# Kernel tuning notes

Measured on AMD Instinct MI355X. Metric: run time of the kernel, lower is better.

Reference implementation:

```python
import jax, jax.numpy as jnp
import numpy as np

N = 50000    # nodes
E = 800000   # edges (avg degree 16)
B = 256      # graphs in the batch (static for segment ops)
H = 128      # feature / hidden width (channels[-2])
NL = 4       # LSTM layers in Set2Set
PS = 4       # Set2Set processing steps
OUT = 2      # channels[-1]


def _bn(h, g, b):
    # BatchNorm1d with batch statistics (training-mode math, biased variance)
    m = h.mean(0)
    v = jnp.mean((h - m) ** 2, 0)
    return (h - m) * jax.lax.rsqrt(v + 1e-5) * g + b


def _gin(x, src, dst, W1, b1, ga1, be1, W2, b2, ga2, be2):
    # GINConv, eps=0: out = MLP(x + sum_{j->i} x_j)
    agg = jax.ops.segment_sum(x[src], dst, num_segments=x.shape[0])
    h = x + agg
    h = jax.nn.relu(_bn(h @ W1.T + b1, ga1, be1))
    h = jax.nn.relu(_bn(h @ W2.T + b2, ga2, be2))
    return h


def _set2set(x, batch, Wih0, Whh0, b0, WihR, WhhR, bR):
    hs = [jnp.zeros((B, H), x.dtype)] * NL
    cs = [jnp.zeros((B, H), x.dtype)] * NL
    q_star = jnp.zeros((B, 2 * H), x.dtype)
    for _ in range(PS):
        inp = q_star
        nhs, ncs = [], []
        for l in range(NL):  # stacked LSTM cells, seq-len 1 per step
            Wih = Wih0 if l == 0 else WihR[l - 1]
            Whh = Whh0 if l == 0 else WhhR[l - 1]
            bb = b0 if l == 0 else bR[l - 1]
            gates = inp @ Wih.T + hs[l] @ Whh.T + bb
            i, f, g, o = jnp.split(gates, 4, axis=-1)  # torch gate order i,f,g,o
            c = jax.nn.sigmoid(f) * cs[l] + jax.nn.sigmoid(i) * jnp.tanh(g)
            h = jax.nn.sigmoid(o) * jnp.tanh(c)
            nhs.append(h); ncs.append(c)
            inp = h
        hs, cs = nhs, ncs
        q = inp  # (B, H) top-layer hidden
        # per-graph segment softmax attention
        e = jnp.sum(x * q[batch], -1)                        # (N,)
        m = jax.ops.segment_max(e, batch, num_segments=B)
        ee = jnp.exp(e - m[batch])
        s = jax.ops.segment_sum(ee, batch, num_segments=B)
        a = ee / s[batch]
        r = jax.ops.segment_sum(a[:, None] * x, batch, num_segments=B)  # (B, H)
        q_star = jnp.concatenate([q, r], -1)
    return q_star


def setup_inputs() -> dict:
    key = jax.random.key(0)
    ks = jax.random.split(key, 16)

    def w(k, shape):
        return jax.random.normal(k, shape, jnp.float32) * 0.05

    d = {}
    d["x"] = jax.random.normal(ks[0], (N, H), jnp.float32)
    d["edge_index"] = jax.random.randint(ks[1], (2, E), 0, N, dtype=jnp.int32)
    d["batch"] = jnp.sort(jax.random.randint(ks[2], (N,), 0, B, dtype=jnp.int32))
    for i, g in enumerate(("g0", "g1")):
        kk = jax.random.split(ks[3 + i], 2)
        d[g + "_W1"] = w(kk[0], (H, H)); d[g + "_b1"] = jnp.zeros((H,), jnp.float32)
        d[g + "_gamma1"] = jnp.ones((H,), jnp.float32); d[g + "_beta1"] = jnp.zeros((H,), jnp.float32)
        d[g + "_W2"] = w(kk[1], (H, H)); d[g + "_b2"] = jnp.zeros((H,), jnp.float32)
        d[g + "_gamma2"] = jnp.ones((H,), jnp.float32); d[g + "_beta2"] = jnp.zeros((H,), jnp.float32)
    d["Wih0"] = w(ks[6], (4 * H, 2 * H))
    d["Whh0"] = w(ks[7], (4 * H, H))
    d["b0"] = jnp.zeros((4 * H,), jnp.float32)
    d["WihR"] = w(ks[8], (NL - 1, 4 * H, H))
    d["WhhR"] = w(ks[9], (NL - 1, 4 * H, H))
    d["bR"] = jnp.zeros((NL - 1, 4 * H), jnp.float32)
    d["lin_W"] = w(ks[10], (OUT, 2 * H))
    d["lin_b"] = jnp.zeros((OUT,), jnp.float32)
    return d


def reference(x, edge_index, batch,
              g0_W1, g0_b1, g0_gamma1, g0_beta1, g0_W2, g0_b2, g0_gamma2, g0_beta2,
              g1_W1, g1_b1, g1_gamma1, g1_beta1, g1_W2, g1_b2, g1_gamma2, g1_beta2,
              Wih0, Whh0, b0, WihR, WhhR, bR, lin_W, lin_b):
    src, dst = edge_index[0], edge_index[1]
    x = _gin(x, src, dst, g0_W1, g0_b1, g0_gamma1, g0_beta1, g0_W2, g0_b2, g0_gamma2, g0_beta2)
    x = _gin(x, src, dst, g1_W1, g1_b1, g1_gamma1, g1_beta1, g1_W2, g1_b2, g1_gamma2, g1_beta2)
    q = _set2set(x, batch, Wih0, Whh0, b0, WihR, WhhR, bR)
    # F.dropout(p=0.1) is identity in eval mode
    return q @ lin_W.T + lin_b
```

## Files before the change

### kernel.cpp

```cpp
#include <hip/hip_runtime.h>
#include <math.h>

#define NN 50000
#define EE 800000
#define BBG 256
#define HHC 128
#define SEG_CAP 448
#define ESC 512
#define NBIN 196
#define NBLK 196

typedef _Float16 half8 __attribute__((ext_vector_type(8)));
typedef _Float16 half4 __attribute__((ext_vector_type(4)));
typedef _Float16 half2v __attribute__((ext_vector_type(2)));
typedef float f32x4 __attribute__((ext_vector_type(4)));

#if defined(__has_builtin)
#if __has_builtin(__builtin_amdgcn_fdot2)
#define USE_FDOT2 1
#endif
#endif

__device__ __forceinline__ float fdot2f(half2v a, half2v b, float c) {
#ifdef USE_FDOT2
  return __builtin_amdgcn_fdot2(a, b, c, false);
#else
  return fmaf((float)a[0], (float)b[0], fmaf((float)a[1], (float)b[1], c));
#endif
}

__device__ __forceinline__ float fsigm(float x) {
  return __builtin_amdgcn_rcpf(1.f + __expf(-x));
}
__device__ __forceinline__ float ftanh(float x) {
  return 1.f - 2.f * __builtin_amdgcn_rcpf(1.f + __expf(2.f * x));
}

__device__ __forceinline__ float4 aff4(float4 v, float4 sc, float4 sh) {
  v.x = fmaxf(fmaf(v.x, sc.x, sh.x), 0.f);
  v.y = fmaxf(fmaf(v.y, sc.y, sh.y), 0.f);
  v.z = fmaxf(fmaf(v.z, sc.z, sh.z), 0.f);
  v.w = fmaxf(fmaf(v.w, sc.w, sh.w), 0.f);
  return v;
}

__global__ __launch_bounds__(256) void prep_all_kernel(
    const int* __restrict__ batch,
    const int* __restrict__ ei,
    const float* __restrict__ W0, const float* __restrict__ W1,
    const float* __restrict__ W2, const float* __restrict__ W3,
    const float* __restrict__ Wih0, const float* __restrict__ Whh0,
    const float* __restrict__ WihR, const float* __restrict__ WhhR,
    const float* __restrict__ b0, const float* __restrict__ bR,
    const float* __restrict__ xsrc,
    float* __restrict__ stats, int* __restrict__ gptr, int* __restrict__ partial,
    _Float16* __restrict__ ginWh, _Float16* __restrict__ WT0h,
    _Float16* __restrict__ WTRh, float* __restrict__ bc0, float* __restrict__ bcR,
    _Float16* __restrict__ x16a) {
  __shared__ int hist[NBIN];
  int blk = blockIdx.x, tid = threadIdx.x;
  if (blk == 0) {
    ((float4*)stats)[tid] = make_float4(0.f, 0.f, 0.f, 0.f);
    return;
  }
  if (blk <= 196) {
    int i = (blk - 1) * 256 + tid;
    if (i >= NN) return;
    int b = batch[i];
    int prev = (i == 0) ? -1 : batch[i - 1];
    for (int g = prev + 1; g <= b; ++g) gptr[g] = i;
    if (i == NN - 1) {
      for (int g = b + 1; g <= BBG; ++g) gptr[g] = NN;
    }
    return;
  }
  if (blk <= 392) {
    int b = blk - 197;
    if (tid < NBIN) hist[tid] = 0;
    __syncthreads();
    const int4* dst4 = (const int4*)(ei + EE);
#pragma unroll
    for (int c = 0; c < 4; ++c) {
      int idx = b * 1024 + c * 256 + tid;
      if (idx < EE / 4) {
        int4 d = dst4[idx];
        atomicAdd(&hist[d.x >> 8], 1);
        atomicAdd(&hist[d.y >> 8], 1);
        atomicAdd(&hist[d.z >> 8], 1);
        atomicAdd(&hist[d.w >> 8], 1);
      }
    }
    __syncthreads();
    if (tid < NBIN) partial[tid * NBLK + b] = hist[tid];
    return;
  }
  if (blk >= 2961) {
    int i = (blk - 2961) * 256 + tid;
    float4 v = ((const float4*)xsrc)[i];
    half4 h;
    h[0] = (_Float16)v.x; h[1] = (_Float16)v.y;
    h[2] = (_Float16)v.z; h[3] = (_Float16)v.w;
    ((half4*)x16a)[i] = h;
    return;
  }
  int idx = (blk - 393) * 256 + tid;
  if (idx < 65536) {
    int m = idx >> 14;
    int r = idx & 16383;
    const float* W = (m == 0) ? W0 : (m == 1) ? W1 : (m == 2) ? W2 : W3;
    ginWh[idx] = (_Float16)W[r];
  } else if (idx < 262144) {
    int t = idx - 65536;
    int k = t >> 9, op = t & 511;
    int j = op >> 2, g = op & 3;
    int row = g * 128 + j;
    float v = (k < 256) ? Wih0[row * 256 + k] : Whh0[row * 128 + (k - 256)];
    WT0h[((k >> 1) << 10) | (op << 1) | (k & 1)] = (_Float16)v;
  } else if (idx < 655360) {
    int t = idx - 262144;
    int l = t >> 17;
    int rem = t & 131071;
    int k = rem >> 9, op = rem & 511;
    int j = op >> 2, g = op & 3;
    int row = g * 128 + j;
    float v = (k < 128) ? WihR[((size_t)l * 512 + row) * 128 + k]
                        : WhhR[((size_t)l * 512 + row) * 128 + (k - 128)];
    WTRh[((size_t)l << 17) | ((k >> 1) << 10) | (op << 1) | (k & 1)] = (_Float16)v;
  } else {
    int t = idx - 655360;
    if (t < 512) {
      bc0[t] = b0[(t & 3) * 128 + (t >> 2)];
    } else {
      int u = t - 512;
      int l = u >> 9, op = u & 511;
      bcR[u] = bR[l * 512 + (op & 3) * 128 + (op >> 2)];
    }
  }
}


__global__ void scan_partials_kernel(const int* __restrict__ partial,
                                     int* __restrict__ block_base, int* __restrict__ total) {
  __shared__ int buf[256];
  int bin = blockIdx.x, tid = threadIdx.x;
  int v = (tid < NBLK) ? partial[bin * NBLK + tid] : 0;
  buf[tid] = v;
  __syncthreads();
  for (int off = 1; off < 256; off <<= 1) {
    int t = (tid >= off) ? buf[tid - off] : 0;
    __syncthreads();
    buf[tid] += t;
    __syncthreads();
  }
  if (tid < NBLK) block_base[bin * NBLK + tid] = buf[tid] - v;
  if (tid == 255) total[bin] = buf[255];
}

__global__ void scan_totals_kernel(const int* __restrict__ total, int* __restrict__ coarse_base) {
  __shared__ int buf[256];
  int tid = threadIdx.x;
  int v = (tid < NBIN) ? total[tid] : 0;
  buf[tid] = v;
  __syncthreads();
  for (int off = 1; off < 256; off <<= 1) {
    int t = (tid >= off) ? buf[tid - off] : 0;
    __syncthreads();
    buf[tid] += t;
    __syncthreads();
  }
  if (tid < NBIN) coarse_base[tid] = buf[tid] - v;
  if (tid == 255) coarse_base[NBIN] = buf[255];
}

__global__ __launch_bounds__(256) void bucket_scatter_kernel(const int* __restrict__ ei,
                                                             const int* __restrict__ coarse_base,
                                                             const int* __restrict__ block_base,
                                                             int* __restrict__ packed) {
  __shared__ int cursor[NBIN];
  int tid = threadIdx.x, b = blockIdx.x;
  if (tid < NBIN) cursor[tid] = coarse_base[tid] + block_base[tid * NBLK + b];
  __syncthreads();
  const int4* src4 = (const int4*)ei;
  const int4* dst4 = (const int4*)(ei + EE);
#pragma unroll
  for (int c = 0; c < 4; ++c) {
    int idx = b * 1024 + c * 256 + tid;
    if (idx < EE / 4) {
      int4 s = src4[idx];
      int4 d = dst4[idx];
      int p;
      p = atomicAdd(&cursor[d.x >> 8], 1); packed[p] = (s.x << 8) | (d.x & 255);
      p = atomicAdd(&cursor[d.y >> 8], 1); packed[p] = (s.y << 8) | (d.y & 255);
      p = atomicAdd(&cursor[d.z >> 8], 1); packed[p] = (s.z << 8) | (d.z & 255);
      p = atomicAdd(&cursor[d.w >> 8], 1); packed[p] = (s.w << 8) | (d.w & 255);
    }
  }
}

__global__ __launch_bounds__(256) void csr_finalize_kernel(const int* __restrict__ packed,
                                                           const int* __restrict__ coarse_base,
                                                           int* __restrict__ row_start,
                                                           int* __restrict__ csr) {
  __shared__ int fh[256];
  __shared__ int fb[256];
  int bin = blockIdx.x, tid = threadIdx.x;
  int e0 = coarse_base[bin], e1 = coarse_base[bin + 1];
  fh[tid] = 0;
  __syncthreads();
  for (int e = e0 + tid; e < e1; e += 256) atomicAdd(&fh[packed[e] & 255], 1);
  __syncthreads();
  int v = fh[tid];
  fb[tid] = v;
  __syncthreads();
  for (int off = 1; off < 256; off <<= 1) {
    int t = (tid >= off) ? fb[tid - off] : 0;
    __syncthreads();
    fb[tid] += t;
    __syncthreads();
  }
  int excl = fb[tid] - v;
  int node = bin * 256 + tid;
  if (node < NN) row_start[node] = e0 + excl;
  if (bin == NBIN - 1 && tid == 0) row_start[NN] = EE;
  __syncthreads();
  fb[tid] = excl;
  __syncthreads();
  for (int e = e0 + tid; e < e1; e += 256) {
    int p = packed[e];
    int pos = atomicAdd(&fb[p & 255], 1);
    csr[e0 + pos] = p >> 8;
  }
}

template <bool AFF>
__global__ __launch_bounds__(256) void gin_agg_kernel(
    const _Float16* __restrict__ x16, const int* __restrict__ row_start,
    const int* __restrict__ csr,
    const float* __restrict__ stats, const float* __restrict__ gamma,
    const float* __restrict__ beta, _Float16* __restrict__ outp) {
  __shared__ float sc_s[128], sh_s[128];
  if (AFF) {
    int tt = threadIdx.x;
    if (tt < 128) {
      const float invN = 1.0f / (float)NN;
      float mm = stats[tt] * invN;
      float vv = stats[128 + tt] * invN - mm * mm;
      float rs = rsqrtf(vv + 1e-5f);
      float sc = gamma[tt] * rs;
      sc_s[tt] = sc;
      sh_s[tt] = beta[tt] - mm * sc;
    }
    __syncthreads();
  }
  int node = blockIdx.x * 4 + (threadIdx.x >> 6);
  int lane = threadIdx.x & 63;
  int q = lane >> 4, t = lane & 15;
  const half8* xh8 = (const half8*)x16;
  float scv[8], shv[8];
  if (AFF) {
#pragma unroll
    for (int f = 0; f < 8; ++f) { scv[f] = sc_s[t * 8 + f]; shv[f] = sh_s[t * 8 + f]; }
  }
  int s0 = row_start[node], s1 = row_start[node + 1];
  float acc[8] = {0.f, 0.f, 0.f, 0.f, 0.f, 0.f, 0.f, 0.f};
  int cnt = s1 - s0;
  int mainEnd = s0 + (cnt & ~15);
  for (int j = s0; j < mainEnd; j += 16) {
    int i0 = csr[j + q + 0];
    int i1 = csr[j + q + 4];
    int i2 = csr[j + q + 8];
    int i3 = csr[j + q + 12];
    half8 h0 = xh8[(size_t)i0 * 16 + t];
    half8 h1 = xh8[(size_t)i1 * 16 + t];
    half8 h2 = xh8[(size_t)i2 * 16 + t];
    half8 h3 = xh8[(size_t)i3 * 16 + t];
    if (AFF) {
#pragma unroll
      for (int f = 0; f < 8; ++f) {
        acc[f] += fmaxf(fmaf((float)h0[f], scv[f], shv[f]), 0.f);
        acc[f] += fmaxf(fmaf((float)h1[f], scv[f], shv[f]), 0.f);
        acc[f] += fmaxf(fmaf((float)h2[f], scv[f], shv[f]), 0.f);
        acc[f] += fmaxf(fmaf((float)h3[f], scv[f], shv[f]), 0.f);
      }
    } else {
#pragma unroll
      for (int f = 0; f < 8; ++f) {
        acc[f] += ((float)h0[f] + (float)h1[f]) + ((float)h2[f] + (float)h3[f]);
      }
    }
  }
  for (int j = mainEnd + q; j < s1; j += 4) {
    int i = csr[j];
    half8 h = xh8[(size_t)i * 16 + t];
    if (AFF) {
#pragma unroll
      for (int f = 0; f < 8; ++f) acc[f] += fmaxf(fmaf((float)h[f], scv[f], shv[f]), 0.f);
    } else {
#pragma unroll
      for (int f = 0; f < 8; ++f) acc[f] += (float)h[f];
    }
  }
#pragma unroll
  for (int f = 0; f < 8; ++f) {
    acc[f] += __shfl_xor(acc[f], 16);
    acc[f] += __shfl_xor(acc[f], 32);
  }
  if (q == 0) {
    half8 selfh = xh8[(size_t)node * 16 + t];
    half8 hv;
#pragma unroll
    for (int f = 0; f < 8; ++f) {
      float sv = (float)selfh[f];
      if (AFF) sv = fmaxf(fmaf(sv, scv[f], shv[f]), 0.f);
      hv[f] = (_Float16)(acc[f] + sv);
    }
    ((half8*)outp)[(size_t)node * 16 + t] = hv;
  }
}

template <bool BN, bool AH>
__global__ __launch_bounds__(256) void gemm_gin_mfma_kernel(
    const float* __restrict__ A, const _Float16* __restrict__ A16,
    const _Float16* __restrict__ Wh,
    const float* __restrict__ bias,
    const float* __restrict__ stats, const float* __restrict__ gamma,
    const float* __restrict__ beta,
    float* __restrict__ C, _Float16* __restrict__ h16out,
    float* __restrict__ ssum, float* __restrict__ ssq) {
  __shared__ float bsc_s[128], bsh_s[128];
  int tid = threadIdx.x;
  if (BN) {
    if (tid < 128) {
      const float invN = 1.0f / (float)NN;
      float mm = stats[tid] * invN;
      float vv = stats[128 + tid] * invN - mm * mm;
      float rs = rsqrtf(vv + 1e-5f);
      float sc = gamma[tid] * rs;
      bsc_s[tid] = sc;
      bsh_s[tid] = beta[tid] - mm * sc;
    }
    __syncthreads();
  }
  int w = tid >> 6, l = tid & 63;
  int lr = l & 15, lg = l >> 4;
  int cb = w * 32;
  half8 bf0[4], bf1[4];
#pragma unroll
  for (int ks = 0; ks < 4; ++ks) {
    int k = ks * 32 + lg * 8;
    bf0[ks] = *(const half8*)(Wh + (size_t)(cb + lr) * 128 + k);
    bf1[ks] = *(const half8*)(Wh + (size_t)(cb + 16 + lr) * 128 + k);
  }
  float bv0 = bias[cb + lr], bv1 = bias[cb + 16 + lr];
  float ps0 = 0.f, pq0 = 0.f, ps1 = 0.f, pq1 = 0.f;
  int t0 = blockIdx.x * 4;
  for (int t = 0; t < 4; ++t) {
    int tile = t0 + t;
    if (tile >= 3125) break;
    int r = tile * 16 + lr;
    half8 af[4];
#pragma unroll
    for (int ks = 0; ks < 4; ++ks) {
      int k0 = ks * 32 + lg * 8;
      if constexpr (AH) {
        half8 ah = *(const half8*)(A16 + (size_t)r * 128 + k0);
        if constexpr (BN) {
          float4 s0 = *(const float4*)&bsc_s[k0];
          float4 s1 = *(const float4*)&bsc_s[k0 + 4];
          float4 h0 = *(const float4*)&bsh_s[k0];
          float4 h1 = *(const float4*)&bsh_s[k0 + 4];
          half8 o;
          o[0] = (_Float16)fmaxf(fmaf((float)ah[0], s0.x, h0.x), 0.f);
          o[1] = (_Float16)fmaxf(fmaf((float)ah[1], s0.y, h0.y), 0.f);
          o[2] = (_Float16)fmaxf(fmaf((float)ah[2], s0.z, h0.z), 0.f);
          o[3] = (_Float16)fmaxf(fmaf((float)ah[3], s0.w, h0.w), 0.f);
          o[4] = (_Float16)fmaxf(fmaf((float)ah[4], s1.x, h1.x), 0.f);
          o[5] = (_Float16)fmaxf(fmaf((float)ah[5], s1.y, h1.y), 0.f);
          o[6] = (_Float16)fmaxf(fmaf((float)ah[6], s1.z, h1.z), 0.f);
          o[7] = (_Float16)fmaxf(fmaf((float)ah[7], s1.w, h1.w), 0.f);
          af[ks] = o;
        } else {
          af[ks] = ah;
        }
      } else {
        float4 a0 = *(const float4*)(A + (size_t)r * 128 + k0);
        float4 a1 = *(const float4*)(A + (size_t)r * 128 + k0 + 4);
        if constexpr (BN) {
          float4 s0 = *(const float4*)&bsc_s[k0];
          float4 s1 = *(const float4*)&bsc_s[k0 + 4];
          float4 h0 = *(const float4*)&bsh_s[k0];
          float4 h1 = *(const float4*)&bsh_s[k0 + 4];
          a0 = aff4(a0, s0, h0);
          a1 = aff4(a1, s1, h1);
        }
        half8 o;
        o[0] = (_Float16)a0.x; o[1] = (_Float16)a0.y;
        o[2] = (_Float16)a0.z; o[3] = (_Float16)a0.w;
        o[4] = (_Float16)a1.x; o[5] = (_Float16)a1.y;
        o[6] = (_Float16)a1.z; o[7] = (_Float16)a1.w;
        af[ks] = o;
      }
    }
    f32x4 acc0 = {0.f, 0.f, 0.f, 0.f};
    f32x4 acc1 = {0.f, 0.f, 0.f, 0.f};
#pragma unroll
    for (int ks = 0; ks < 4; ++ks) {
      acc0 = __builtin_amdgcn_mfma_f32_16x16x32_f16(af[ks], bf0[ks], acc0, 0, 0, 0);
      acc1 = __builtin_amdgcn_mfma_f32_16x16x32_f16(af[ks], bf1[ks], acc1, 0, 0, 0);
    }
#pragma unroll
    for (int i = 0; i < 4; ++i) {
      int rr = tile * 16 + lg * 4 + i;
      float v0 = acc0[i] + bv0;
      float v1 = acc1[i] + bv1;
      if (C) {
        C[(size_t)rr * 128 + cb + lr] = v0;
        C[(size_t)rr * 128 + cb + 16 + lr] = v1;
      }
      if (h16out) {
        h16out[(size_t)rr * 128 + cb + lr] = (_Float16)v0;
        h16out[(size_t)rr * 128 + cb + 16 + lr] = (_Float16)v1;
      }
      ps0 += v0; pq0 += v0 * v0;
      ps1 += v1; pq1 += v1 * v1;
    }
  }
  ps0 += __shfl_xor(ps0, 16); ps0 += __shfl_xor(ps0, 32);
  pq0 += __shfl_xor(pq0, 16); pq0 += __shfl_xor(pq0, 32);
  ps1 += __shfl_xor(ps1, 16); ps1 += __shfl_xor(ps1, 32);
  pq1 += __shfl_xor(pq1, 16); pq1 += __shfl_xor(pq1, 32);
  if (lg == 0) {
    atomicAdd(&ssum[cb + lr], ps0);
    atomicAdd(&ssq[cb + lr], pq0);
    atomicAdd(&ssum[cb + 16 + lr], ps1);
    atomicAdd(&ssq[cb + 16 + lr], pq1);
  }
}

__global__ void __launch_bounds__(1024) set2set_kernel(
    const float* __restrict__ x, const int* __restrict__ gptr,
    const float* __restrict__ stats, const float* __restrict__ gamma,
    const float* __restrict__ beta,
    const _Float16* __restrict__ WT0h, const _Float16* __restrict__ WTRh,
    const float* __restrict__ bc0, const float* __restrict__ bcR,
    float* __restrict__ ebuf,
    const float* __restrict__ linW, const float* __restrict__ linb,
    float* __restrict__ out) {
  __shared__ half2v xs[SEG_CAP * 64];
  __shared__ float wpart[16][512];
  __shared__ half2v inp2[192];
  __shared__ float hcs[4][128];
  __shared__ float ccs[4][128];
  __shared__ float qst[256];
  __shared__ float es[ESC];
  __shared__ float bsc[128], bsh[128];
  __shared__ float wred[16];
  __shared__ float smax_s, ssum_s;
  __shared__ float fred[2][4];

  int g = blockIdx.x, tid = threadIdx.x;
  int w16 = tid >> 6, lane = tid & 63;

  if (tid < 128) {
    const float invN = 1.0f / (float)NN;
    float mm = stats[tid] * invN;
    float vv = stats[128 + tid] * invN - mm * mm;
    float rs = rsqrtf(vv + 1e-5f);
    float sc = gamma[tid] * rs;
    bsc[tid] = sc;
    bsh[tid] = beta[tid] - mm * sc;
#pragma unroll
    for (int l = 0; l < 4; ++l) { hcs[l][tid] = 0.f; ccs[l][tid] = 0.f; }
  }
  if (tid < 256) qst[tid] = 0.f;
  __syncthreads();

  int s0 = gptr[g], s1 = gptr[g + 1];
  int seg = s1 - s0;
  int ncache = seg < SEG_CAP ? seg : SEG_CAP;
  const float2* x2 = (const float2*)x;
  float sc0 = bsc[2 * lane], sc1 = bsc[2 * lane + 1];
  float sh0 = bsh[2 * lane], sh1 = bsh[2 * lane + 1];
  for (int n = w16; n < ncache; n += 16) {
    float2 v = x2[(size_t)(s0 + n) * 64 + lane];
    half2v h;
    h[0] = (_Float16)fmaxf(fmaf(v.x, sc0, sh0), 0.f);
    h[1] = (_Float16)fmaxf(fmaf(v.y, sc1, sh1), 0.f);
    xs[n * 64 + lane] = h;
  }
  __syncthreads();

  int s_ = tid >> 6, cg = tid & 63;

  for (int step = 0; step < 4; ++step) {
    for (int cell = 0; cell < 4; ++cell) {
      const _Float16* WTh; const float* bias; int KP2;
      if (cell == 0) {
        WTh = WT0h; bias = bc0; KP2 = 12;
        if (tid < 192) {
          int k = tid << 1;
          float va, vb;
          if (k < 256) { va = qst[k]; vb = qst[k + 1]; }
          else { va = hcs[0][k - 256]; vb = hcs[0][k - 255]; }
          half2v h; h[0] = (_Float16)va; h[1] = (_Float16)vb;
          inp2[tid] = h;
        }
      } else {
        WTh = WTRh + (size_t)(cell - 1) * 131072;
        bias = bcR + (cell - 1) * 512; KP2 = 8;
        if (tid < 128) {
          int k = tid << 1;
          float va, vb;
          if (k < 128) { va = hcs[cell - 1][k]; vb = hcs[cell - 1][k + 1]; }
          else { va = hcs[cell][k - 128]; vb = hcs[cell][k - 127]; }
          half2v h; h[0] = (_Float16)va; h[1] = (_Float16)vb;
          inp2[tid] = h;
        }
      }
      __syncthreads();
      bool skipmv = (step == 0 && cell == 0);
      if (!skipmv) {
        int se = (s_ + g) & 15;
        int k20 = se * KP2;
        float a0 = 0.f, a1 = 0.f, a2 = 0.f, a3 = 0.f;
        float a4 = 0.f, a5 = 0.f, a6 = 0.f, a7 = 0.f;
        if (step != 0 || se < 8) {
          const char* wb = (const char*)WTh + (size_t)k20 * 2048 + (cg << 5);
#pragma unroll 4
          for (int k2 = 0; k2 < KP2; ++k2) {
            uint4 wa = *(const uint4*)(wb + (size_t)k2 * 2048);
            uint4 wc = *(const uint4*)(wb + (size_t)k2 * 2048 + 16);
            half2v i2 = inp2[k20 + k2];
            a0 = fdot2f(i2, __builtin_bit_cast(half2v, wa.x), a0);
            a1 = fdot2f(i2, __builtin_bit_cast(half2v, wa.y), a1);
            a2 = fdot2f(i2, __builtin_bit_cast(half2v, wa.z), a2);
            a3 = fdot2f(i2, __builtin_bit_cast(half2v, wa.w), a3);
            a4 = fdot2f(i2, __builtin_bit_cast(half2v, wc.x), a4);
            a5 = fdot2f(i2, __builtin_bit_cast(half2v, wc.y), a5);
            a6 = fdot2f(i2, __builtin_bit_cast(half2v, wc.z), a6);
            a7 = fdot2f(i2, __builtin_bit_cast(half2v, wc.w), a7);
          }
        }
        *(float4*)&wpart[s_][cg << 3] = make_float4(a0, a1, a2, a3);
        *(float4*)(&wpart[s_][cg << 3] + 4) = make_float4(a4, a5, a6, a7);
        __syncthreads();
      }
      if (tid < 128) {
        int j = tid;
        float4 ga = *(const float4*)&bias[4 * j];
        if (!skipmv) {
#pragma unroll
          for (int s = 0; s < 16; ++s) {
            float4 wv = *(const float4*)&wpart[s][4 * j];
            ga.x += wv.x; ga.y += wv.y; ga.z += wv.z; ga.w += wv.w;
          }
        }
        float cp = ccs[cell][j];
        float si = fsigm(ga.x);
        float sf = fsigm(ga.y);
        float so = fsigm(ga.w);
        float cn = sf * cp + si * ftanh(ga.z);
        ccs[cell][j] = cn;
        hcs[cell][j] = so * ftanh(cn);
      }
      __syncthreads();
    }
    float* rpart = &wpart[0][0];
    float qx = hcs[3][2 * lane], qy = hcs[3][2 * lane + 1];
    half2v q2; q2[0] = (_Float16)qx; q2[1] = (_Float16)qy;
    float wmax = -3.0e38f;
    for (int n = w16; n < seg; n += 16) {
      float e;
      if (n < ncache) {
        e = fdot2f(xs[n * 64 + lane], q2, 0.f);
      } else {
        float2 v = x2[(size_t)(s0 + n) * 64 + lane];
        float vx = fmaxf(fmaf(v.x, sc0, sh0), 0.f);
        float vy = fmaxf(fmaf(v.y, sc1, sh1), 0.f);
        e = vx * qx + vy * qy;
      }
#pragma unroll
      for (int sh = 32; sh; sh >>= 1) e += __shfl_xor(e, sh);
      if (lane == 0) { if (n < ESC) es[n] = e; else ebuf[s0 + n] = e; }
      wmax = fmaxf(wmax, e);
    }
    if (lane == 0) wred[w16] = wmax;
    __syncthreads();
    if (tid == 0) {
      float m = wred[0];
#pragma unroll
      for (int t = 1; t < 16; ++t) m = fmaxf(m, wred[t]);
      smax_s = m;
    }
    __syncthreads();
    float m = smax_s;
    float loc = 0.f;
    for (int n = tid; n < seg; n += 1024) {
      float e = (n < ESC) ? es[n] : ebuf[s0 + n];
      float ex = __expf(e - m);
      if (n < ESC) es[n] = ex; else ebuf[s0 + n] = ex;
      loc += ex;
    }
#pragma unroll
    for (int sh = 32; sh; sh >>= 1) loc += __shfl_xor(loc, sh);
    __syncthreads();
    if (lane == 0) wred[w16] = loc;
    __syncthreads();
    if (tid == 0) {
      float s = 0.f;
#pragma unroll
      for (int t = 0; t < 16; ++t) s += wred[t];
      ssum_s = s;
    }
    __syncthreads();
    float inv = 1.0f / ssum_s;
    float rx = 0.f, ry = 0.f;
    for (int n = w16; n < seg; n += 16) {
      float ex = (n < ESC) ? es[n] : ebuf[s0 + n];
      float coef = ex * inv;
      float vx, vy;
      if (n < ncache) {
        half2v v2 = xs[n * 64 + lane];
        vx = (float)v2[0]; vy = (float)v2[1];
      } else {
        float2 v = x2[(size_t)(s0 + n) * 64 + lane];
        vx = fmaxf(fmaf(v.x, sc0, sh0), 0.f);
        vy = fmaxf(fmaf(v.y, sc1, sh1), 0.f);
      }
      rx += coef * vx; ry += coef * vy;
    }
    rpart[w16 * 128 + 2 * lane] = rx;
    rpart[w16 * 128 + 2 * lane + 1] = ry;
    __syncthreads();
    if (tid < 128) {
      float r = 0.f;
#pragma unroll
      for (int t = 0; t < 16; ++t) r += rpart[t * 128 + tid];
      qst[tid] = hcs[3][tid];
      qst[128 + tid] = r;
    }
    __syncthreads();
  }
  if (tid < 256) {
    float val = qst[tid];
    float p0 = val * linW[tid];
    float p1 = val * linW[256 + tid];
#pragma unroll
    for (int sh = 32; sh; sh >>= 1) { p0 += __shfl_xor(p0, sh); p1 += __shfl_xor(p1, sh); }
    if (lane == 0) { fred[0][w16] = p0; fred[1][w16] = p1; }
  }
  __syncthreads();
  if (tid == 0) {
    out[2 * g + 0] = fred[0][0] + fred[0][1] + fred[0][2] + fred[0][3] + linb[0];
    out[2 * g + 1] = fred[1][0] + fred[1][1] + fred[1][2] + fred[1][3] + linb[1];
  }
}


extern "C" void kernel_launch(void* const* d_in, const int* in_sizes, int n_in,
                              void* d_out, int out_size, void* d_ws, size_t ws_size,
                              hipStream_t stream) {
  const float* x = (const float*)d_in[0];
  const int* ei = (const int*)d_in[1];
  const int* batch = (const int*)d_in[2];
  const float* gW[4]  = {(const float*)d_in[3],  (const float*)d_in[7],
                         (const float*)d_in[11], (const float*)d_in[15]};
  const float* gb[4]  = {(const float*)d_in[4],  (const float*)d_in[8],
                         (const float*)d_in[12], (const float*)d_in[16]};
  const float* gga[4] = {(const float*)d_in[5],  (const float*)d_in[9],
                         (const float*)d_in[13], (const float*)d_in[17]};
  const float* gbe[4] = {(const float*)d_in[6],  (const float*)d_in[10],
                         (const float*)d_in[14], (const float*)d_in[18]};
  const float* Wih0 = (const float*)d_in[19];
  const float* Whh0 = (const float*)d_in[20];
  const float* b0   = (const float*)d_in[21];
  const float* WihR = (const float*)d_in[22];
  const float* WhhR = (const float*)d_in[23];
  const float* bR   = (const float*)d_in[24];
  const float* linW = (const float*)d_in[25];
  const float* linb = (const float*)d_in[26];
  float* out = (float*)d_out;

  char* base = (char*)d_ws;
  size_t off = 0;
  auto allocf = [&](size_t n) { float* p = (float*)(base + off); off += n * sizeof(float); return p; };
  float* xa    = allocf(6400000);
  _Float16* agg16 = (_Float16*)(base + off); off += 6400000 * 2;
  _Float16* ginWh = (_Float16*)(base + off); off += 65536 * 2;
  _Float16* WT0h = (_Float16*)(base + off); off += 196608 * 2;
  _Float16* WTRh = (_Float16*)(base + off); off += 393216 * 2;
  _Float16* x16a = (_Float16*)(base + off); off += 6400000 * 2;
  _Float16* x16b = (_Float16*)(base + off); off += 6400000 * 2;
  float* bc0   = allocf(512);
  float* bcR   = allocf(1536);
  float* ebuf  = allocf(50000);
  float* stats = allocf(1024);
  int* row_start = (int*)(base + off); off += 50004 * 4;
  int* gptr = (int*)(base + off); off += 260 * 4;
  int* csr = (int*)(base + off); off += 800000 * 4;
  int* packed = (int*)(base + off); off += 800000 * 4;
  int* partial = (int*)(base + off); off += NBIN * NBLK * 4;
  int* block_base = (int*)(base + off); off += NBIN * NBLK * 4;
  int* total = (int*)(base + off); off += 256 * 4;
  int* coarse_base = (int*)(base + off); off += 260 * 4;
  (void)ws_size; (void)in_sizes; (void)n_in; (void)out_size;

  prep_all_kernel<<<9211, 256, 0, stream>>>(batch, ei, gW[0], gW[1], gW[2], gW[3],
                                            Wih0, Whh0, WihR, WhhR, b0, bR, x,
                                            stats, gptr, partial, ginWh, WT0h, WTRh,
                                            bc0, bcR, x16a);
  scan_partials_kernel<<<NBIN, 256, 0, stream>>>(partial, block_base, total);
  scan_totals_kernel<<<1, 256, 0, stream>>>(total, coarse_base);
  bucket_scatter_kernel<<<NBLK, 256, 0, stream>>>(ei, coarse_base, block_base, packed);
  csr_finalize_kernel<<<NBIN, 256, 0, stream>>>(packed, coarse_base, row_start, csr);

  gin_agg_kernel<false><<<12500, 256, 0, stream>>>(x16a, row_start, csr,
                                                   nullptr, nullptr, nullptr, agg16);
  gemm_gin_mfma_kernel<false, true><<<782, 256, 0, stream>>>(
      nullptr, agg16, ginWh + 0 * 16384, gb[0],
      nullptr, nullptr, nullptr,
      nullptr, x16a, stats + 0, stats + 128);
  gemm_gin_mfma_kernel<true, true><<<782, 256, 0, stream>>>(
      nullptr, x16a, ginWh + 1 * 16384, gb[1],
      stats + 0, gga[0], gbe[0],
      nullptr, x16b, stats + 256, stats + 384);
  gin_agg_kernel<true><<<12500, 256, 0, stream>>>(x16b, row_start, csr,
                                                  stats + 256, gga[1], gbe[1], agg16);
  gemm_gin_mfma_kernel<false, true><<<782, 256, 0, stream>>>(
      nullptr, agg16, ginWh + 2 * 16384, gb[2],
      nullptr, nullptr, nullptr,
      nullptr, x16a, stats + 512, stats + 640);
  gemm_gin_mfma_kernel<true, true><<<782, 256, 0, stream>>>(
      nullptr, x16a, ginWh + 3 * 16384, gb[3],
      stats + 512, gga[2], gbe[2],
      xa, nullptr, stats + 768, stats + 896);

  set2set_kernel<<<256, 1024, 0, stream>>>(xa, gptr, stats + 768, gga[3], gbe[3],
                                           WT0h, WTRh, bc0, bcR, ebuf, linW, linb, out);
}
```

Baseline: 425.4 us.

## Assign one 16-lane group per node in GIN aggregation and pass fp16 features to Set2Set

The GIN aggregation kernel now gives each node 16 lanes instead of a full 64-lane wavefront. Each group walks its edge list serially with an 8-way unroll, which removes the cross-quarter shuffle reduction and the idle lanes on low-degree nodes. The last GEMM now writes fp16 output instead of fp32, and Set2Set reads half-precision features, which halves its global read traffic and removes the fp32 buffer. The risks are reduced memory-level parallelism per node and slightly lower precision of the Set2Set input.

```diff
diff --git a/kernel.cpp b/kernel.cpp
--- a/kernel.cpp
+++ b/kernel.cpp
@@ -233,6 +233,17 @@
 }
 
 template <bool AFF>
+__device__ __forceinline__ void acc8(float* acc, half8 h, const float* scv,
+                                     const float* shv) {
+#pragma unroll
+  for (int f = 0; f < 8; ++f) {
+    float v = (float)h[f];
+    if (AFF) v = fmaxf(fmaf(v, scv[f], shv[f]), 0.f);
+    acc[f] += v;
+  }
+}
+
+template <bool AFF>
 __global__ __launch_bounds__(256) void gin_agg_kernel(
     const _Float16* __restrict__ x16, const int* __restrict__ row_start,
     const int* __restrict__ csr,
@@ -252,9 +263,8 @@
     }
     __syncthreads();
   }
-  int node = blockIdx.x * 4 + (threadIdx.x >> 6);
-  int lane = threadIdx.x & 63;
-  int q = lane >> 4, t = lane & 15;
+  int node = blockIdx.x * 16 + (threadIdx.x >> 4);
+  int t = threadIdx.x & 15;
   const half8* xh8 = (const half8*)x16;
   float scv[8], shv[8];
   if (AFF) {
@@ -263,59 +273,62 @@
   }
   int s0 = row_start[node], s1 = row_start[node + 1];
   float acc[8] = {0.f, 0.f, 0.f, 0.f, 0.f, 0.f, 0.f, 0.f};
-  int cnt = s1 - s0;
-  int mainEnd = s0 + (cnt & ~15);
-  for (int j = s0; j < mainEnd; j += 16) {
-    int i0 = csr[j + q + 0];
-    int i1 = csr[j + q + 4];
-    int i2 = csr[j + q + 8];
-    int i3 = csr[j + q + 12];
+  int j = s0;
+  for (; j + 8 <= s1; j += 8) {
+    int i0 = csr[j + 0];
+    int i1 = csr[j + 1];
+    int i2 = csr[j + 2];
+    int i3 = csr[j + 3];
+    int i4 = csr[j + 4];
+    int i5 = csr[j + 5];
+    int i6 = csr[j + 6];
+    int i7 = csr[j + 7];
     half8 h0 = xh8[(size_t)i0 * 16 + t];
     half8 h1 = xh8[(size_t)i1 * 16 + t];
     half8 h2 = xh8[(size_t)i2 * 16 + t];
     half8 h3 = xh8[(size_t)i3 * 16 + t];
-    if (AFF) {
-#pragma unroll
-      for (int f = 0; f < 8; ++f) {
-        acc[f] += fmaxf(fmaf((float)h0[f], scv[f], shv[f]), 0.f);
-        acc[f] += fmaxf(fmaf((float)h1[f], scv[f], shv[f]), 0.f);
-        acc[f] += fmaxf(fmaf((float)h2[f], scv[f], shv[f]), 0.f);
-        acc[f] += fmaxf(fmaf((float)h3[f], scv[f], shv[f]), 0.f);
-      }
-    } else {
-#pragma unroll
-      for (int f = 0; f < 8; ++f) {
-        acc[f] += ((float)h0[f] + (float)h1[f]) + ((float)h2[f] + (float)h3[f]);
-      }
-    }
-  }
-  for (int j = mainEnd + q; j < s1; j += 4) {
+    half8 h4 = xh8[(size_t)i4 * 16 + t];
+    half8 h5 = xh8[(size_t)i5 * 16 + t];
+    half8 h6 = xh8[(size_t)i6 * 16 + t];
+    half8 h7 = xh8[(size_t)i7 * 16 + t];
+    acc8<AFF>(acc, h0, scv, shv);
+    acc8<AFF>(acc, h1, scv, shv);
+    acc8<AFF>(acc, h2, scv, shv);
+    acc8<AFF>(acc, h3, scv, shv);
+    acc8<AFF>(acc, h4, scv, shv);
+    acc8<AFF>(acc, h5, scv, shv);
+    acc8<AFF>(acc, h6, scv, shv);
+    acc8<AFF>(acc, h7, scv, shv);
+  }
+  if (j + 4 <= s1) {
+    int i0 = csr[j + 0];
+    int i1 = csr[j + 1];
+    int i2 = csr[j + 2];
+    int i3 = csr[j + 3];
+    half8 h0 = xh8[(size_t)i0 * 16 + t];
+    half8 h1 = xh8[(size_t)i1 * 16 + t];
+    half8 h2 = xh8[(size_t)i2 * 16 + t];
+    half8 h3 = xh8[(size_t)i3 * 16 + t];
+    acc8<AFF>(acc, h0, scv, shv);
+    acc8<AFF>(acc, h1, scv, shv);
+    acc8<AFF>(acc, h2, scv, shv);
+    acc8<AFF>(acc, h3, scv, shv);
+    j += 4;
+  }
+  for (; j < s1; ++j) {
     int i = csr[j];
     half8 h = xh8[(size_t)i * 16 + t];
-    if (AFF) {
-#pragma unroll
-      for (int f = 0; f < 8; ++f) acc[f] += fmaxf(fmaf((float)h[f], scv[f], shv[f]), 0.f);
-    } else {
-#pragma unroll
-      for (int f = 0; f < 8; ++f) acc[f] += (float)h[f];
-    }
-  }
+    acc8<AFF>(acc, h, scv, shv);
+  }
+  half8 selfh = xh8[(size_t)node * 16 + t];
+  half8 hv;
 #pragma unroll
   for (int f = 0; f < 8; ++f) {
-    acc[f] += __shfl_xor(acc[f], 16);
-    acc[f] += __shfl_xor(acc[f], 32);
-  }
-  if (q == 0) {
-    half8 selfh = xh8[(size_t)node * 16 + t];
-    half8 hv;
-#pragma unroll
-    for (int f = 0; f < 8; ++f) {
-      float sv = (float)selfh[f];
-      if (AFF) sv = fmaxf(fmaf(sv, scv[f], shv[f]), 0.f);
-      hv[f] = (_Float16)(acc[f] + sv);
-    }
-    ((half8*)outp)[(size_t)node * 16 + t] = hv;
-  }
+    float sv = (float)selfh[f];
+    if (AFF) sv = fmaxf(fmaf(sv, scv[f], shv[f]), 0.f);
+    hv[f] = (_Float16)(acc[f] + sv);
+  }
+  ((half8*)outp)[(size_t)node * 16 + t] = hv;
 }
 
 template <bool BN, bool AH>
@@ -438,7 +451,7 @@
 }
 
 __global__ void __launch_bounds__(1024) set2set_kernel(
-    const float* __restrict__ x, const int* __restrict__ gptr,
+    const _Float16* __restrict__ x, const int* __restrict__ gptr,
     const float* __restrict__ stats, const float* __restrict__ gamma,
     const float* __restrict__ beta,
     const _Float16* __restrict__ WT0h, const _Float16* __restrict__ WTRh,
@@ -478,14 +491,14 @@
   int s0 = gptr[g], s1 = gptr[g + 1];
   int seg = s1 - s0;
   int ncache = seg < SEG_CAP ? seg : SEG_CAP;
-  const float2* x2 = (const float2*)x;
+  const half2v* xh = (const half2v*)x;
   float sc0 = bsc[2 * lane], sc1 = bsc[2 * lane + 1];
   float sh0 = bsh[2 * lane], sh1 = bsh[2 * lane + 1];
   for (int n = w16; n < ncache; n += 16) {
-    float2 v = x2[(size_t)(s0 + n) * 64 + lane];
+    half2v v = xh[(size_t)(s0 + n) * 64 + lane];
     half2v h;
-    h[0] = (_Float16)fmaxf(fmaf(v.x, sc0, sh0), 0.f);
-    h[1] = (_Float16)fmaxf(fmaf(v.y, sc1, sh1), 0.f);
+    h[0] = (_Float16)fmaxf(fmaf((float)v[0], sc0, sh0), 0.f);
+    h[1] = (_Float16)fmaxf(fmaf((float)v[1], sc1, sh1), 0.f);
     xs[n * 64 + lane] = h;
   }
   __syncthreads();
@@ -574,9 +587,9 @@
       if (n < ncache) {
         e = fdot2f(xs[n * 64 + lane], q2, 0.f);
       } else {
-        float2 v = x2[(size_t)(s0 + n) * 64 + lane];
-        float vx = fmaxf(fmaf(v.x, sc0, sh0), 0.f);
-        float vy = fmaxf(fmaf(v.y, sc1, sh1), 0.f);
+        half2v v = xh[(size_t)(s0 + n) * 64 + lane];
+        float vx = fmaxf(fmaf((float)v[0], sc0, sh0), 0.f);
+        float vy = fmaxf(fmaf((float)v[1], sc1, sh1), 0.f);
         e = vx * qx + vy * qy;
       }
 #pragma unroll
@@ -623,9 +636,9 @@
         half2v v2 = xs[n * 64 + lane];
         vx = (float)v2[0]; vy = (float)v2[1];
       } else {
-        float2 v = x2[(size_t)(s0 + n) * 64 + lane];
-        vx = fmaxf(fmaf(v.x, sc0, sh0), 0.f);
-        vy = fmaxf(fmaf(v.y, sc1, sh1), 0.f);
+        half2v v = xh[(size_t)(s0 + n) * 64 + lane];
+        vx = fmaxf(fmaf((float)v[0], sc0, sh0), 0.f);
+        vy = fmaxf(fmaf((float)v[1], sc1, sh1), 0.f);
       }
       rx += coef * vx; ry += coef * vy;
     }
@@ -684,7 +697,6 @@
   char* base = (char*)d_ws;
   size_t off = 0;
   auto allocf = [&](size_t n) { float* p = (float*)(base + off); off += n * sizeof(float); return p; };
-  float* xa    = allocf(6400000);
   _Float16* agg16 = (_Float16*)(base + off); off += 6400000 * 2;
   _Float16* ginWh = (_Float16*)(base + off); off += 65536 * 2;
   _Float16* WT0h = (_Float16*)(base + off); off += 196608 * 2;
@@ -714,8 +726,8 @@
   bucket_scatter_kernel<<<NBLK, 256, 0, stream>>>(ei, coarse_base, block_base, packed);
   csr_finalize_kernel<<<NBIN, 256, 0, stream>>>(packed, coarse_base, row_start, csr);
 
-  gin_agg_kernel<false><<<12500, 256, 0, stream>>>(x16a, row_start, csr,
-                                                   nullptr, nullptr, nullptr, agg16);
+  gin_agg_kernel<false><<<3125, 256, 0, stream>>>(x16a, row_start, csr,
+                                                  nullptr, nullptr, nullptr, agg16);
   gemm_gin_mfma_kernel<false, true><<<782, 256, 0, stream>>>(
       nullptr, agg16, ginWh + 0 * 16384, gb[0],
       nullptr, nullptr, nullptr,
@@ -724,8 +736,8 @@
       nullptr, x16a, ginWh + 1 * 16384, gb[1],
       stats + 0, gga[0], gbe[0],
       nullptr, x16b, stats + 256, stats + 384);
-  gin_agg_kernel<true><<<12500, 256, 0, stream>>>(x16b, row_start, csr,
-                                                  stats + 256, gga[1], gbe[1], agg16);
+  gin_agg_kernel<true><<<3125, 256, 0, stream>>>(x16b, row_start, csr,
+                                                 stats + 256, gga[1], gbe[1], agg16);
   gemm_gin_mfma_kernel<false, true><<<782, 256, 0, stream>>>(
       nullptr, agg16, ginWh + 2 * 16384, gb[2],
       nullptr, nullptr, nullptr,
@@ -733,8 +745,8 @@
   gemm_gin_mfma_kernel<true, true><<<782, 256, 0, stream>>>(
       nullptr, x16a, ginWh + 3 * 16384, gb[3],
       stats + 512, gga[2], gbe[2],
-      xa, nullptr, stats + 768, stats + 896);
-
-  set2set_kernel<<<256, 1024, 0, stream>>>(xa, gptr, stats + 768, gga[3], gbe[3],
+      nullptr, x16b, stats + 768, stats + 896);
+
+  set2set_kernel<<<256, 1024, 0, stream>>>(x16b, gptr, stats + 768, gga[3], gbe[3],
                                            WT0h, WTRh, bc0, bcR, ebuf, linW, linb, out);
 }
```

Result: no change. 424.2 us (-0.3%).
